# Performance work log

Hardware: AMD Instinct MI355X
Metric: run time of the kernel (lower is better)

Reference implementation:

```python
import jax, jax.numpy as jnp
import numpy as np

D = 2          # in_out_dim
HID = 64       # hidden_dim of hypernet
WIDTH = 64     # number of rank-1 blocks
COND = 4       # condition_dim
BATCH = 262144
BLOCK = WIDTH * D


def setup_inputs() -> dict:
    key = jax.random.key(0)
    ks = jax.random.split(key, 8)
    s = lambda k, shape, scale: (jax.random.normal(k, shape, jnp.float32) * scale)
    return {
        "t": jax.random.uniform(ks[0], (1,), jnp.float32),
        "z": jax.random.normal(ks[1], (BATCH, D), jnp.float32),
        "logp_z": jnp.zeros((BATCH, 1), jnp.float32),
        "condition": jax.random.normal(ks[2], (BATCH, COND), jnp.float32),
        # HyperNetwork params (torch Linear convention: weight [out, in])
        "hn_w1": s(ks[3], (HID, 1), 1.0), "hn_b1": jnp.zeros((HID,), jnp.float32),
        "hn_w2": s(ks[4], (HID, HID), 1.0 / np.sqrt(HID)), "hn_b2": jnp.zeros((HID,), jnp.float32),
        "hn_w3": s(ks[5], (3 * BLOCK + WIDTH, HID), 1.0 / np.sqrt(HID)), "hn_b3": jnp.zeros((3 * BLOCK + WIDTH,), jnp.float32),
        # TanhSigmoidMultiplyCondition params
        "cl_wz": s(ks[6], (2 * D, D), 1.0 / np.sqrt(D)), "cl_bz": jnp.zeros((2 * D,), jnp.float32),
        "cl_wc": s(ks[7], (2 * D, COND), 1.0 / np.sqrt(COND)), "cl_bc": jnp.zeros((2 * D,), jnp.float32),
    }


def reference(t, z, logp_z, condition, hn_w1, hn_b1, hn_w2, hn_b2, hn_w3, hn_b3,
              cl_wz, cl_bz, cl_wc, cl_bc):
    # --- TanhSigmoidMultiplyCondition: gated fusion of z and condition ---
    in_act = z @ cl_wz.T + cl_bz + condition @ cl_wc.T + cl_bc   # [B, 2D]
    zc = jnp.tanh(in_act[:, :D]) * jax.nn.sigmoid(in_act[:, D:])  # [B, D]

    # --- HyperNetwork: t -> per-block weights W, B, U ---
    p = jnp.tanh(t.reshape(1, 1) @ hn_w1.T + hn_b1)
    p = jnp.tanh(p @ hn_w2.T + hn_b2)
    p = (p @ hn_w3.T + hn_b3).reshape(-1)          # [3*BLOCK + WIDTH]
    W = p[:BLOCK].reshape(WIDTH, D, 1)
    U = p[BLOCK:2 * BLOCK].reshape(WIDTH, 1, D)
    G = p[2 * BLOCK:3 * BLOCK].reshape(WIDTH, 1, D)
    U = U * jax.nn.sigmoid(G)
    Bb = p[3 * BLOCK:].reshape(WIDTH, 1, 1)

    def f(zz):  # velocity field dz/dt as a function of the conditioned z
        h = jnp.tanh(jnp.einsum('bd,wdo->wbo', zz, W) + Bb)  # [WIDTH, B, 1]
        return jnp.einsum('wbo,wod->bd', h, U) / WIDTH        # mean over WIDTH -> [B, D]

    dz_dt = f(zc)

    # trace of Jacobian d(dz_dt)/d(zc) via forward-mode JVPs over the D basis vectors
    eye = jnp.eye(D, dtype=zc.dtype)
    tangents = jax.vmap(
        lambda e: jax.jvp(f, (zc,), (jnp.broadcast_to(e, zc.shape),))[1]
    )(eye)                                   # [D, B, D]
    trace = jnp.einsum('ibi->b', tangents)   # sum of diagonal entries
    dlogp_z_dt = -trace.reshape(-1, 1)       # [B, 1]

    return (dz_dt, dlogp_z_dt, condition)
```

## Files before the change

kernel.cpp:

```cpp
#include <hip/hip_runtime.h>
#include <math.h>

#define D 2
#define HID 64
#define WIDTH 64
#define CONDDIM 4
#define BATCH 262144
#define BLK 128

static __device__ __forceinline__ float fexp2(float x){ return __builtin_amdgcn_exp2f(x); }
static __device__ __forceinline__ float frcp(float x){ return __builtin_amdgcn_rcpf(x); }

__global__ __launch_bounds__(448) void hyper_kernel(
    const float* __restrict__ t,
    const float* __restrict__ w1, const float* __restrict__ b1,
    const float* __restrict__ w2, const float* __restrict__ b2,
    const float* __restrict__ w3, const float* __restrict__ b3,
    float* __restrict__ params)
{
    __shared__ float p1s[HID];
    __shared__ float p2s[HID];
    __shared__ float p3s[3*BLK + WIDTH];
    const int tid = threadIdx.x;

    if (tid < HID) p1s[tid] = tanhf(t[0]*w1[tid] + b1[tid]);
    __syncthreads();

    if (tid < HID) {
        float acc = b2[tid];
        const float* row = w2 + tid*HID;
        #pragma unroll 8
        for (int k = 0; k < HID; ++k) acc = fmaf(p1s[k], row[k], acc);
        p2s[tid] = tanhf(acc);
    }
    __syncthreads();

    {
        float a0=0.f, a1=0.f, a2=0.f, a3=0.f;
        const float* row = w3 + tid*HID;
        #pragma unroll 4
        for (int k = 0; k < HID; k += 4) {
            a0 = fmaf(p2s[k+0], row[k+0], a0);
            a1 = fmaf(p2s[k+1], row[k+1], a1);
            a2 = fmaf(p2s[k+2], row[k+2], a2);
            a3 = fmaf(p2s[k+3], row[k+3], a3);
        }
        p3s[tid] = b3[tid] + ((a0+a1)+(a2+a3));
    }
    __syncthreads();

    if (tid < WIDTH) {
        const int w = tid;
        const float C = 2.885390081777927f;
        float W0 = p3s[2*w],        W1 = p3s[2*w+1];
        float U0 = p3s[BLK+2*w],    U1 = p3s[BLK+2*w+1];
        float G0 = p3s[2*BLK+2*w],  G1 = p3s[2*BLK+2*w+1];
        float Bb = p3s[3*BLK+w];
        U0 *= 1.0f/(1.0f + expf(-G0));
        U1 *= 1.0f/(1.0f + expf(-G1));
        float Us0 = U0 * (1.0f/WIDTH);
        float Us1 = U1 * (1.0f/WIDTH);
        float WUs = W0*Us0 + W1*Us1;
        params[8*w+0] = W0*C;
        params[8*w+1] = W1*C;
        params[8*w+2] = Bb*C;
        params[8*w+3] = WUs;
        params[8*w+4] = Us0;
        params[8*w+5] = Us1;
        params[8*w+6] = 0.0f;
        params[8*w+7] = 0.0f;
        float s = WUs;
        #pragma unroll
        for (int off = 32; off > 0; off >>= 1) s += __shfl_down(s, off);
        if (w == 0) params[512] = s;
    }
}

__global__ __launch_bounds__(256) void ode_kernel(
    const float4* __restrict__ z4,
    const float4* __restrict__ c4,
    const float* __restrict__ cl_wz, const float* __restrict__ cl_bz,
    const float* __restrict__ cl_wc, const float* __restrict__ cl_bc,
    const float* __restrict__ params,
    float* __restrict__ out)
{
    const int gid = blockIdx.x * 256 + threadIdx.x;
    const float L2E = 1.4426950408889634f;
    const float C2  = 2.885390081777927f;

    float wz[8], wc[16], bb[4];
    #pragma unroll
    for (int j = 0; j < 8;  ++j) wz[j] = cl_wz[j];
    #pragma unroll
    for (int j = 0; j < 16; ++j) wc[j] = cl_wc[j];
    #pragma unroll
    for (int j = 0; j < 4;  ++j) bb[j] = cl_bz[j] + cl_bc[j];

    float4 zz = z4[gid];
    float4 cA = c4[2*gid];
    float4 cB = c4[2*gid+1];

    float a[4], b[4];
    #pragma unroll
    for (int j = 0; j < 4; ++j) {
        float ta = fmaf(zz.x, wz[2*j], fmaf(zz.y, wz[2*j+1], bb[j]));
        ta = fmaf(cA.x, wc[4*j], ta); ta = fmaf(cA.y, wc[4*j+1], ta);
        ta = fmaf(cA.z, wc[4*j+2], ta); ta = fmaf(cA.w, wc[4*j+3], ta);
        a[j] = ta;
        float tb = fmaf(zz.z, wz[2*j], fmaf(zz.w, wz[2*j+1], bb[j]));
        tb = fmaf(cB.x, wc[4*j], tb); tb = fmaf(cB.y, wc[4*j+1], tb);
        tb = fmaf(cB.z, wc[4*j+2], tb); tb = fmaf(cB.w, wc[4*j+3], tb);
        b[j] = tb;
    }
    float zc0A = fmaf(-2.0f, frcp(1.0f + fexp2(a[0]*C2)), 1.0f) * frcp(1.0f + fexp2(-a[2]*L2E));
    float zc1A = fmaf(-2.0f, frcp(1.0f + fexp2(a[1]*C2)), 1.0f) * frcp(1.0f + fexp2(-a[3]*L2E));
    float zc0B = fmaf(-2.0f, frcp(1.0f + fexp2(b[0]*C2)), 1.0f) * frcp(1.0f + fexp2(-b[2]*L2E));
    float zc1B = fmaf(-2.0f, frcp(1.0f + fexp2(b[1]*C2)), 1.0f) * frcp(1.0f + fexp2(-b[3]*L2E));

    const float4* __restrict__ P = (const float4*)params;
    float acc0A=0.f, acc1A=0.f, trA=0.f;
    float acc0B=0.f, acc1B=0.f, trB=0.f;
    #pragma unroll 8
    for (int w = 0; w < WIDTH; ++w) {
        float4 pa = P[2*w];
        float4 pb = P[2*w+1];
        float preA = fmaf(pa.x, zc0A, fmaf(pa.y, zc1A, pa.z));
        float preB = fmaf(pa.x, zc0B, fmaf(pa.y, zc1B, pa.z));
        float hA = fmaf(-2.0f, frcp(1.0f + fexp2(preA)), 1.0f);
        float hB = fmaf(-2.0f, frcp(1.0f + fexp2(preB)), 1.0f);
        acc0A = fmaf(hA, pb.x, acc0A);  acc1A = fmaf(hA, pb.y, acc1A);
        acc0B = fmaf(hB, pb.x, acc0B);  acc1B = fmaf(hB, pb.y, acc1B);
        trA = fmaf(hA*hA, pa.w, trA);
        trB = fmaf(hB*hB, pa.w, trB);
    }
    float sWU = params[512];

    ((float4*)out)[gid] = make_float4(acc0A, acc1A, acc0B, acc1B);
    ((float2*)(out + 2*(size_t)BATCH))[gid] = make_float2(trA - sWU, trB - sWU);
    float4* oc = (float4*)(out + 3*(size_t)BATCH);
    oc[2*gid]   = cA;
    oc[2*gid+1] = cB;
}

extern "C" void kernel_launch(void* const* d_in, const int* in_sizes, int n_in,
                              void* d_out, int out_size, void* d_ws, size_t ws_size,
                              hipStream_t stream) {
    const float* t         = (const float*)d_in[0];
    const float* z         = (const float*)d_in[1];
    const float* condition = (const float*)d_in[3];
    const float* hn_w1 = (const float*)d_in[4];
    const float* hn_b1 = (const float*)d_in[5];
    const float* hn_w2 = (const float*)d_in[6];
    const float* hn_b2 = (const float*)d_in[7];
    const float* hn_w3 = (const float*)d_in[8];
    const float* hn_b3 = (const float*)d_in[9];
    const float* cl_wz = (const float*)d_in[10];
    const float* cl_bz = (const float*)d_in[11];
    const float* cl_wc = (const float*)d_in[12];
    const float* cl_bc = (const float*)d_in[13];

    float* params = (float*)d_ws;

    hyper_kernel<<<1, 448, 0, stream>>>(t, hn_w1, hn_b1, hn_w2, hn_b2, hn_w3, hn_b3, params);

    const int nthreads = BATCH / 2;
    const int block = 256;
    const int grid = nthreads / block;
    ode_kernel<<<grid, block, 0, stream>>>((const float4*)z, (const float4*)condition,
                                           cl_wz, cl_bz, cl_wc, cl_bc, params, (float*)d_out);
}
```

Measured before the change: 22.34 us.

## Fuse hypernetwork into ODE kernel, recomputing params per block in shared memory

Removes the separate single-block hypernetwork launch: every block of the ODE kernel now recomputes the hypernetwork MLP (64x64 and 448x64 matvecs) into shared memory, then reads params from LDS instead of global memory. This eliminates a kernel launch and the serialization between the tiny first kernel and the main kernel. In exchange each of 512 blocks redoes ~30K FMAs and reads ~130KB of weights (cached in L2), adding barriers and a prologue before the main per-sample work. The condition copy-out store is also moved earlier to overlap with compute.

```diff
diff --git a/kernel.cpp b/kernel.cpp
--- a/kernel.cpp
+++ b/kernel.cpp
@@ -11,82 +11,30 @@
 static __device__ __forceinline__ float fexp2(float x){ return __builtin_amdgcn_exp2f(x); }
 static __device__ __forceinline__ float frcp(float x){ return __builtin_amdgcn_rcpf(x); }
 
-__global__ __launch_bounds__(448) void hyper_kernel(
+__global__ __launch_bounds__(256) void fused_ode_kernel(
     const float* __restrict__ t,
-    const float* __restrict__ w1, const float* __restrict__ b1,
-    const float* __restrict__ w2, const float* __restrict__ b2,
-    const float* __restrict__ w3, const float* __restrict__ b3,
-    float* __restrict__ params)
+    const float* __restrict__ hw1, const float* __restrict__ hb1,
+    const float* __restrict__ hw2, const float* __restrict__ hb2,
+    const float* __restrict__ hw3, const float* __restrict__ hb3,
+    const float4* __restrict__ z4,
+    const float4* __restrict__ c4,
+    const float* __restrict__ cl_wz, const float* __restrict__ cl_bz,
+    const float* __restrict__ cl_wc, const float* __restrict__ cl_bc,
+    float* __restrict__ out)
 {
     __shared__ float p1s[HID];
     __shared__ float p2s[HID];
     __shared__ float p3s[3*BLK + WIDTH];
+    __shared__ __align__(16) float ps[520];
+
     const int tid = threadIdx.x;
-
-    if (tid < HID) p1s[tid] = tanhf(t[0]*w1[tid] + b1[tid]);
-    __syncthreads();
-
-    if (tid < HID) {
-        float acc = b2[tid];
-        const float* row = w2 + tid*HID;
-        #pragma unroll 8
-        for (int k = 0; k < HID; ++k) acc = fmaf(p1s[k], row[k], acc);
-        p2s[tid] = tanhf(acc);
-    }
-    __syncthreads();
-
-    {
-        float a0=0.f, a1=0.f, a2=0.f, a3=0.f;
-        const float* row = w3 + tid*HID;
-        #pragma unroll 4
-        for (int k = 0; k < HID; k += 4) {
-            a0 = fmaf(p2s[k+0], row[k+0], a0);
-            a1 = fmaf(p2s[k+1], row[k+1], a1);
-            a2 = fmaf(p2s[k+2], row[k+2], a2);
-            a3 = fmaf(p2s[k+3], row[k+3], a3);
-        }
-        p3s[tid] = b3[tid] + ((a0+a1)+(a2+a3));
-    }
-    __syncthreads();
-
-    if (tid < WIDTH) {
-        const int w = tid;
-        const float C = 2.885390081777927f;
-        float W0 = p3s[2*w],        W1 = p3s[2*w+1];
-        float U0 = p3s[BLK+2*w],    U1 = p3s[BLK+2*w+1];
-        float G0 = p3s[2*BLK+2*w],  G1 = p3s[2*BLK+2*w+1];
-        float Bb = p3s[3*BLK+w];
-        U0 *= 1.0f/(1.0f + expf(-G0));
-        U1 *= 1.0f/(1.0f + expf(-G1));
-        float Us0 = U0 * (1.0f/WIDTH);
-        float Us1 = U1 * (1.0f/WIDTH);
-        float WUs = W0*Us0 + W1*Us1;
-        params[8*w+0] = W0*C;
-        params[8*w+1] = W1*C;
-        params[8*w+2] = Bb*C;
-        params[8*w+3] = WUs;
-        params[8*w+4] = Us0;
-        params[8*w+5] = Us1;
-        params[8*w+6] = 0.0f;
-        params[8*w+7] = 0.0f;
-        float s = WUs;
-        #pragma unroll
-        for (int off = 32; off > 0; off >>= 1) s += __shfl_down(s, off);
-        if (w == 0) params[512] = s;
-    }
-}
-
-__global__ __launch_bounds__(256) void ode_kernel(
-    const float4* __restrict__ z4,
-    const float4* __restrict__ c4,
-    const float* __restrict__ cl_wz, const float* __restrict__ cl_bz,
-    const float* __restrict__ cl_wc, const float* __restrict__ cl_bc,
-    const float* __restrict__ params,
-    float* __restrict__ out)
-{
-    const int gid = blockIdx.x * 256 + threadIdx.x;
+    const int gid = blockIdx.x * 256 + tid;
     const float L2E = 1.4426950408889634f;
     const float C2  = 2.885390081777927f;
+
+    float4 zz = z4[gid];
+    float4 cA = c4[2*gid];
+    float4 cB = c4[2*gid+1];
 
     float wz[8], wc[16], bb[4];
     #pragma unroll
@@ -96,9 +44,81 @@
     #pragma unroll
     for (int j = 0; j < 4;  ++j) bb[j] = cl_bz[j] + cl_bc[j];
 
-    float4 zz = z4[gid];
-    float4 cA = c4[2*gid];
-    float4 cB = c4[2*gid+1];
+    if (tid < HID) p1s[tid] = tanhf(t[0]*hw1[tid] + hb1[tid]);
+    __syncthreads();
+
+    if (tid < HID) {
+        float a0=0.f, a1=0.f, a2=0.f, a3=0.f;
+        const float4* row = (const float4*)(hw2 + tid*HID);
+        #pragma unroll 4
+        for (int k = 0; k < HID/4; ++k) {
+            float4 r = row[k];
+            a0 = fmaf(p1s[4*k+0], r.x, a0);
+            a1 = fmaf(p1s[4*k+1], r.y, a1);
+            a2 = fmaf(p1s[4*k+2], r.z, a2);
+            a3 = fmaf(p1s[4*k+3], r.w, a3);
+        }
+        p2s[tid] = tanhf(hb2[tid] + ((a0+a1)+(a2+a3)));
+    }
+    __syncthreads();
+
+    {
+        int r = tid;
+        {
+            float a0=0.f, a1=0.f, a2=0.f, a3=0.f;
+            const float4* row = (const float4*)(hw3 + r*HID);
+            #pragma unroll 4
+            for (int k = 0; k < HID/4; ++k) {
+                float4 rv = row[k];
+                a0 = fmaf(p2s[4*k+0], rv.x, a0);
+                a1 = fmaf(p2s[4*k+1], rv.y, a1);
+                a2 = fmaf(p2s[4*k+2], rv.z, a2);
+                a3 = fmaf(p2s[4*k+3], rv.w, a3);
+            }
+            p3s[r] = hb3[r] + ((a0+a1)+(a2+a3));
+        }
+        if (tid < 192) {
+            int r2 = 256 + tid;
+            float a0=0.f, a1=0.f, a2=0.f, a3=0.f;
+            const float4* row = (const float4*)(hw3 + r2*HID);
+            #pragma unroll 4
+            for (int k = 0; k < HID/4; ++k) {
+                float4 rv = row[k];
+                a0 = fmaf(p2s[4*k+0], rv.x, a0);
+                a1 = fmaf(p2s[4*k+1], rv.y, a1);
+                a2 = fmaf(p2s[4*k+2], rv.z, a2);
+                a3 = fmaf(p2s[4*k+3], rv.w, a3);
+            }
+            p3s[r2] = hb3[r2] + ((a0+a1)+(a2+a3));
+        }
+    }
+    __syncthreads();
+
+    if (tid < WIDTH) {
+        const int w = tid;
+        float W0 = p3s[2*w],        W1 = p3s[2*w+1];
+        float U0 = p3s[BLK+2*w],    U1 = p3s[BLK+2*w+1];
+        float G0 = p3s[2*BLK+2*w],  G1 = p3s[2*BLK+2*w+1];
+        float Bb = p3s[3*BLK+w];
+        U0 *= frcp(1.0f + fexp2(-G0*L2E));
+        U1 *= frcp(1.0f + fexp2(-G1*L2E));
+        float Us0 = U0 * (1.0f/WIDTH);
+        float Us1 = U1 * (1.0f/WIDTH);
+        float WUs = W0*Us0 + W1*Us1;
+        ps[8*w+0] = W0*C2;
+        ps[8*w+1] = W1*C2;
+        ps[8*w+2] = Bb*C2;
+        ps[8*w+3] = WUs;
+        ps[8*w+4] = Us0;
+        ps[8*w+5] = Us1;
+        ps[8*w+6] = 0.0f;
+        ps[8*w+7] = 0.0f;
+        float s = WUs;
+        #pragma unroll
+        for (int off = 32; off > 0; off >>= 1) s += __shfl_down(s, off);
+        if (w == 0) ps[512] = s;
+    }
+    __syncthreads();
 
     float a[4], b[4];
     #pragma unroll
@@ -117,7 +137,11 @@
     float zc0B = fmaf(-2.0f, frcp(1.0f + fexp2(b[0]*C2)), 1.0f) * frcp(1.0f + fexp2(-b[2]*L2E));
     float zc1B = fmaf(-2.0f, frcp(1.0f + fexp2(b[1]*C2)), 1.0f) * frcp(1.0f + fexp2(-b[3]*L2E));
 
-    const float4* __restrict__ P = (const float4*)params;
+    float4* oc = (float4*)(out + 3*(size_t)BATCH);
+    oc[2*gid]   = cA;
+    oc[2*gid+1] = cB;
+
+    const float4* __restrict__ P = (const float4*)ps;
     float acc0A=0.f, acc1A=0.f, trA=0.f;
     float acc0B=0.f, acc1B=0.f, trB=0.f;
     #pragma unroll 8
@@ -133,13 +157,10 @@
         trA = fmaf(hA*hA, pa.w, trA);
         trB = fmaf(hB*hB, pa.w, trB);
     }
-    float sWU = params[512];
+    float sWU = ps[512];
 
     ((float4*)out)[gid] = make_float4(acc0A, acc1A, acc0B, acc1B);
     ((float2*)(out + 2*(size_t)BATCH))[gid] = make_float2(trA - sWU, trB - sWU);
-    float4* oc = (float4*)(out + 3*(size_t)BATCH);
-    oc[2*gid]   = cA;
-    oc[2*gid+1] = cB;
 }
 
 extern "C" void kernel_launch(void* const* d_in, const int* in_sizes, int n_in,
@@ -159,13 +180,11 @@
     const float* cl_wc = (const float*)d_in[12];
     const float* cl_bc = (const float*)d_in[13];
 
-    float* params = (float*)d_ws;
-
-    hyper_kernel<<<1, 448, 0, stream>>>(t, hn_w1, hn_b1, hn_w2, hn_b2, hn_w3, hn_b3, params);
-
     const int nthreads = BATCH / 2;
     const int block = 256;
     const int grid = nthreads / block;
-    ode_kernel<<<grid, block, 0, stream>>>((const float4*)z, (const float4*)condition,
-                                           cl_wz, cl_bz, cl_wc, cl_bc, params, (float*)d_out);
+    fused_ode_kernel<<<grid, block, 0, stream>>>(
+        t, hn_w1, hn_b1, hn_w2, hn_b2, hn_w3, hn_b3,
+        (const float4*)z, (const float4*)condition,
+        cl_wz, cl_bz, cl_wc, cl_bc, (float*)d_out);
 }
```

Measured after the change: 20.84 us. 1.07x faster.
